# Kernel optimization log

Measured on AMD Instinct MI355X. Metric: run time of the kernel, lower is better.

The kernel has to match this reference:

```python
import jax, jax.numpy as jnp
import numpy as np

DIM = 1024
NUM_HEADS = 16
HEAD_DIM = DIM // NUM_HEADS  # 64
T = 4096
ATTN_SCALE = 0.12


def _rope_tables(t, head_dim):
    # angular_freq: (1/1024)**linspace(0,1,head_dim//4), then zeros for head_dim//4 -> head_dim//2
    af = (1.0 / 1024.0) ** jnp.linspace(0.0, 1.0, head_dim // 4, dtype=jnp.float32)
    af = jnp.concatenate([af, jnp.zeros(head_dim // 4, dtype=jnp.float32)])
    theta = jnp.arange(t, dtype=jnp.float32)[:, None] * af[None, :]  # [T, head_dim//2]
    return jnp.cos(theta), jnp.sin(theta)


def _rms_norm(x):
    eps = jnp.finfo(jnp.float32).eps
    ms = jnp.mean(jnp.square(x.astype(jnp.float32)), axis=-1, keepdims=True)
    return (x * jax.lax.rsqrt(ms + eps)).astype(x.dtype)


def _rotary(x, cos, sin):
    # x: [B, T, H, D]; cos/sin: [T, D//2]
    xf = x.astype(jnp.float32)
    x1, x2 = jnp.split(xf, 2, axis=-1)
    c = cos[None, :, None, :]
    s = sin[None, :, None, :]
    y1 = x1 * c + x2 * s
    y2 = -x1 * s + x2 * c
    return jnp.concatenate([y1, y2], axis=-1).astype(x.dtype)


def setup_inputs() -> dict:
    key = jax.random.key(0)
    k1, k2, k3, k4 = jax.random.split(key, 4)
    std = 0.5 * DIM ** (-0.5)
    bound = (3.0 ** 0.5) * std
    x = jax.random.normal(k1, (1, T, DIM), dtype=jnp.float32)
    ve = jax.random.normal(k2, (1, T, DIM), dtype=jnp.float32)
    qkv_w = jax.random.uniform(k3, (3, DIM, DIM), dtype=jnp.float32, minval=-bound, maxval=bound)
    lambdas = jnp.array([0.5, 0.5], dtype=jnp.float32)
    # source zero-inits c_proj; use random weights for a non-degenerate baseline
    c_proj_w = jax.random.uniform(k4, (DIM, DIM), dtype=jnp.float32, minval=-bound, maxval=bound)
    return {"x": x, "ve": ve, "qkv_w": qkv_w, "lambdas": lambdas, "c_proj_w": c_proj_w}


def reference(x, ve, qkv_w, lambdas, c_proj_w):
    B, t, _ = x.shape
    # fused QKV: F.linear(x, qkv_w.flatten(end_dim=1)) -> [B, T, 3*dim]
    qkv = jnp.einsum('btd,ed->bte', x, qkv_w.reshape(3 * DIM, DIM))
    qkv = qkv.reshape(B, t, 3 * NUM_HEADS, HEAD_DIM)
    q, k, v = jnp.split(qkv, 3, axis=-2)  # each [B, T, H, Dh]
    # lambda-weighted value-embedding mix
    v = lambdas[0] * v + lambdas[1] * ve.reshape(B, t, NUM_HEADS, HEAD_DIM)
    # RMSNorm per head, then RoPE
    q, k = _rms_norm(q), _rms_norm(k)
    cos, sin = _rope_tables(t, HEAD_DIM)
    q, k = _rotary(q, cos, sin), _rotary(k, cos, sin)
    # causal attention with fixed scale (flex_attention w/ causal block mask)
    scores = jnp.einsum('bqhd,bkhd->bhqk', q, k) * ATTN_SCALE
    causal = jnp.tril(jnp.ones((t, t), dtype=bool))
    scores = jnp.where(causal[None, None], scores, jnp.finfo(scores.dtype).min)
    probs = jax.nn.softmax(scores, axis=-1)
    y = jnp.einsum('bhqk,bkhd->bqhd', probs, v).reshape(B, t, DIM)
    return jnp.einsum('btd,ed->bte', y, c_proj_w)
```

## Files before the change

### kernel.cpp

```cpp
#include <hip/hip_runtime.h>
#include <stdint.h>


typedef __attribute__((ext_vector_type(8))) __bf16 bf16x8;
typedef __attribute__((ext_vector_type(8))) unsigned short u16x8;
typedef __attribute__((ext_vector_type(4))) float f32x4;
typedef __attribute__((ext_vector_type(16))) float f32x16;

union U8 { u16x8 s; bf16x8 b; };
union PF { unsigned int u[4]; u16x8 s; bf16x8 b; };

__device__ __forceinline__ float bf2f(unsigned short u) {
  union { unsigned int i; float f; } c; c.i = ((unsigned int)u) << 16; return c.f;
}
__device__ __forceinline__ unsigned short f2bf(float f) {
  union { __bf16 h; unsigned short u; } c; c.h = (__bf16)f; return c.u;
}
__device__ __forceinline__ unsigned int pk2(float lo, float hi) {
  return (unsigned int)f2bf(lo) | ((unsigned int)f2bf(hi) << 16);
}

#define GLOAD16(gp, lp)                                                         \
  __builtin_amdgcn_global_load_lds(                                             \
      (const __attribute__((address_space(1))) void*)(gp),                      \
      (__attribute__((address_space(3))) void*)(lp), 16, 0, 0)

#define MFMA16(a, b, c) __builtin_amdgcn_mfma_f32_16x16x32_bf16((a), (b), (c), 0, 0, 0)
#define MFMA32(a, b, c) __builtin_amdgcn_mfma_f32_32x32x16_bf16((a), (b), (c), 0, 0, 0)

constexpr float ATTN_SCALE = 0.12f;
constexpr float LOG2E = 1.44269504088896340736f;
constexpr float QSCALE = ATTN_SCALE * LOG2E;
constexpr float MFIX = 12.0f;

__global__ void rope_tab(float* __restrict__ ct, float* __restrict__ st) {
  const int i = blockIdx.x * 256 + threadIdx.x;
  if (i >= 4096 * 32) return;
  const int tt = i >> 5, k = i & 31;
  float cv = 1.0f, sv = 0.0f;
  if (k < 16) {
    const float af = powf(1.0f / 1024.0f, (float)k * (1.0f / 15.0f));
    const float th = (float)tt * af;
    cv = cosf(th);
    sv = sinf(th);
  }
  ct[i] = cv; st[i] = sv;
}

__global__ void cast_f2b8(const float* __restrict__ in, unsigned short* __restrict__ out, int n8) {
  const int i = blockIdx.x * 256 + threadIdx.x;
  if (i >= n8) return;
  const float4 a = ((const float4*)in)[2 * i];
  const float4 b = ((const float4*)in)[2 * i + 1];
  u16x8 o;
  o[0] = f2bf(a.x); o[1] = f2bf(a.y); o[2] = f2bf(a.z); o[3] = f2bf(a.w);
  o[4] = f2bf(b.x); o[5] = f2bf(b.y); o[6] = f2bf(b.z); o[7] = f2bf(b.w);
  ((u16x8*)out)[i] = o;
}

template <int OUT_BF16>
__global__ __launch_bounds__(256) void gemm_bt(
    const unsigned short* __restrict__ A, const unsigned short* __restrict__ B,
    void* __restrict__ Cout, int M, int N, int K) {
  __shared__ unsigned short lA[128 * 32];
  __shared__ unsigned short lB[128 * 32];
  const int nbn = N >> 7;
  const int bm = blockIdx.x / nbn, bn = blockIdx.x % nbn;
  const int t = threadIdx.x;
  const int w = t >> 6, l = t & 63;
  const int g = l >> 4, c = l & 15;
  const int wr = (w >> 1) * 64, wc = (w & 1) * 64;

  const int srow = t >> 2;
  const int scol = ((t & 3) << 4) ^ ((srow & 3) << 4);
  const char* ga = (const char*)(A + (size_t)(bm * 128 + srow) * K) + scol;
  const char* gb = (const char*)(B + (size_t)(bn * 128 + srow) * K) + scol;
  const size_t rowK2 = (size_t)64 * K * 2;
  char* la_dst = (char*)lA + t * 16;
  char* lb_dst = (char*)lB + t * 16;

  f32x4 acc[4][4] = {};

  for (int kt = 0; kt < K; kt += 32) {
    const char* gak = ga + (size_t)kt * 2;
    const char* gbk = gb + (size_t)kt * 2;
    GLOAD16(gak, la_dst);
    GLOAD16(gak + rowK2, la_dst + 4096);
    GLOAD16(gbk, lb_dst);
    GLOAD16(gbk + rowK2, lb_dst + 4096);
    __syncthreads();
    U8 af[4], bfr[4];
#pragma unroll
    for (int mi = 0; mi < 4; ++mi) {
      const int row = wr + 16 * mi + c;
      af[mi].s = *(const u16x8*)((const char*)lA + row * 64 + ((16 * g) ^ ((row & 3) << 4)));
    }
#pragma unroll
    for (int ni = 0; ni < 4; ++ni) {
      const int row = wc + 16 * ni + c;
      bfr[ni].s = *(const u16x8*)((const char*)lB + row * 64 + ((16 * g) ^ ((row & 3) << 4)));
    }
#pragma unroll
    for (int mi = 0; mi < 4; ++mi)
#pragma unroll
      for (int ni = 0; ni < 4; ++ni)
        acc[mi][ni] = MFMA16(af[mi].b, bfr[ni].b, acc[mi][ni]);
    __syncthreads();
  }
#pragma unroll
  for (int mi = 0; mi < 4; ++mi) {
#pragma unroll
    for (int ni = 0; ni < 4; ++ni) {
#pragma unroll
      for (int r = 0; r < 4; ++r) {
        const int row = bm * 128 + wr + 16 * mi + 4 * g + r;
        const int col = bn * 128 + wc + 16 * ni + c;
        const float v = acc[mi][ni][r];
        if (OUT_BF16)
          ((unsigned short*)Cout)[(size_t)row * N + col] = f2bf(v);
        else
          ((float*)Cout)[(size_t)row * N + col] = v;
      }
    }
  }
}

__device__ __forceinline__ void load64f(const unsigned short* p, float* x) {
#pragma unroll
  for (int j = 0; j < 8; ++j) {
    const u16x8 v = *(const u16x8*)(p + 8 * j);
#pragma unroll
    for (int e = 0; e < 8; ++e) x[8 * j + e] = bf2f(v[e]);
  }
}

__device__ __forceinline__ void rmsrope_store_blk(const float* x, const float* ct,
                                                  const float* st, unsigned short* outp,
                                                  float pscale) {
  float ms = 0.f;
#pragma unroll
  for (int j = 0; j < 64; ++j) ms += x[j] * x[j];
  const float sc = rsqrtf(ms * (1.0f / 64.0f) + 1.1920928955078125e-7f) * pscale;
  float y[64];
#pragma unroll
  for (int j = 0; j < 32; ++j) {
    const float cc = ct[j], ss = st[j];
    const float a = x[j] * sc, b = x[j + 32] * sc;
    y[j] = a * cc + b * ss;
    y[j + 32] = b * cc - a * ss;
  }
#pragma unroll
  for (int j = 0; j < 8; ++j) {
    u16x8 o;
#pragma unroll
    for (int e = 0; e < 8; ++e) o[e] = f2bf(y[8 * j + e]);
    *(u16x8*)(outp + 256 * j) = o;
  }
}

__global__ __launch_bounds__(256) void fuse_qkv(
    const unsigned short* __restrict__ qkv,
    const float* __restrict__ ve,
    const float* __restrict__ lam,
    const float* __restrict__ ct, const float* __restrict__ st,
    unsigned short* __restrict__ Qb,
    unsigned short* __restrict__ Kb,
    unsigned short* __restrict__ Vb)
{
  __shared__ unsigned short vtile[8][32][65];
  const int b = (int)blockIdx.x;
  const int h = b & 15, tg = b >> 4;
  const int t = threadIdx.x;
  const int g = t >> 5, lq = t & 31;
  const int ti = tg * 8 + g;
  const int tt = ti * 32 + lq;

  const unsigned short* base = qkv + (size_t)tt * 3072 + h * 64;
  const float* ctp = ct + tt * 32;
  const float* stp = st + tt * 32;
  const size_t blk = (size_t)h * 262144 + (size_t)ti * 2048 + lq * 8;

  float x[64];
  load64f(base, x);
  rmsrope_store_blk(x, ctp, stp, Qb + blk, QSCALE);
  load64f(base + 1024, x);
  rmsrope_store_blk(x, ctp, stp, Kb + blk, 1.0f);

  const float l0 = lam[0], l1 = lam[1];
  const float* vp = ve + (size_t)tt * 1024 + h * 64;
  load64f(base + 2048, x);
#pragma unroll
  for (int j = 0; j < 64; ++j) vtile[g][lq][j] = f2bf(l0 * x[j] + l1 * vp[j]);
  __syncthreads();

  unsigned short* vo = Vb + (size_t)h * 262144 + (size_t)ti * 2048 + lq * 8;
#pragma unroll
  for (int r = 0; r < 4; ++r) {
    const int d = lq + 32 * (r & 1);
#pragma unroll
    for (int hi = 0; hi < 2; ++hi) {
      u16x8 o;
#pragma unroll
      for (int j = 0; j < 8; ++j) o[j] = vtile[g][16 * (r >> 1) + 8 * hi + j][d];
      *(u16x8*)(vo + r * 512 + hi * 256) = o;
    }
  }
}

__global__ __launch_bounds__(256, 4) void attn_fa(
    const unsigned short* __restrict__ Qb,
    const unsigned short* __restrict__ Kb,
    const unsigned short* __restrict__ Vb,
    unsigned short* __restrict__ Y)
{
  __shared__ unsigned short oLb[4][64][32];
  __shared__ float sumL[4][32];

  const int b = (int)blockIdx.x;
  const int h = 2 * (b & 7) + ((b >> 3) & 1);
  const int qb = 127 - (b >> 4);
  const int q0 = qb * 32;
  const int t = threadIdx.x;
  const int w = t >> 6, l = t & 63;
  const int lq = l & 31;
  const int hi = l >> 5;

  const unsigned short* kh = Kb + (size_t)h * 262144 + l * 8;
  const unsigned short* vh = Vb + (size_t)h * 262144 + l * 8;

  U8 qf[4];
  {
    const unsigned short* qp = Qb + (size_t)h * 262144 + qb * 2048 + l * 8;
#pragma unroll
    for (int dd = 0; dd < 4; ++dd) qf[dd].s = *(const u16x8*)(qp + dd * 512);
  }

  U8 onesf;
#pragma unroll
  for (int e = 0; e < 8; ++e) onesf.s[e] = 0x3F80;

  f32x16 o0 = {}, o1 = {};
  f32x16 osum = {};

  for (int ti = w; ti <= qb; ti += 4) {
    const unsigned short* kp = kh + ti * 2048;
    const unsigned short* vp = vh + ti * 2048;
    U8 kf[4], vf[4];
#pragma unroll
    for (int dd = 0; dd < 4; ++dd) kf[dd].s = *(const u16x8*)(kp + dd * 512);
#pragma unroll
    for (int r = 0; r < 4; ++r) vf[r].s = *(const u16x8*)(vp + r * 512);

    __builtin_amdgcn_s_setprio(1);
    f32x16 s0 = {};
#pragma unroll
    for (int dd = 0; dd < 4; ++dd) s0 = MFMA32(kf[dd].b, qf[dd].b, s0);
    __builtin_amdgcn_s_setprio(0);

    if (ti == qb) {
      const int thr0 = lq - 4 * hi;
#pragma unroll
      for (int e = 0; e < 16; ++e) {
        const int kvr = (e & 3) + 8 * (e >> 2);
        if (kvr > thr0) s0[e] = -3e38f;
      }
    }

#pragma unroll
    for (int e = 0; e < 16; ++e) s0[e] = exp2f(s0[e] - MFIX);

#define DO_SLAB(KS)                                                              \
  do {                                                                           \
    const unsigned int ua = pk2(s0[8 * (KS) + 0], s0[8 * (KS) + 1]);             \
    const unsigned int ub = pk2(s0[8 * (KS) + 2], s0[8 * (KS) + 3]);             \
    const unsigned int uc = pk2(s0[8 * (KS) + 4], s0[8 * (KS) + 5]);             \
    const unsigned int ud = pk2(s0[8 * (KS) + 6], s0[8 * (KS) + 7]);             \
    const unsigned int sa = (unsigned int)__shfl_xor((int)ua, 32);               \
    const unsigned int sb = (unsigned int)__shfl_xor((int)ub, 32);               \
    const unsigned int sc = (unsigned int)__shfl_xor((int)uc, 32);               \
    const unsigned int sd = (unsigned int)__shfl_xor((int)ud, 32);               \
    PF pf;                                                                       \
    pf.u[0] = hi ? sc : ua;                                                      \
    pf.u[1] = hi ? sd : ub;                                                      \
    pf.u[2] = hi ? uc : sa;                                                      \
    pf.u[3] = hi ? ud : sb;                                                      \
    __builtin_amdgcn_s_setprio(1);                                               \
    o0 = MFMA32(vf[2 * (KS)].b, pf.b, o0);                                       \
    o1 = MFMA32(vf[2 * (KS) + 1].b, pf.b, o1);                                   \
    osum = MFMA32(onesf.b, pf.b, osum);                                          \
    __builtin_amdgcn_s_setprio(0);                                               \
  } while (0)

    DO_SLAB(0);
    DO_SLAB(1);
#undef DO_SLAB
  }

#pragma unroll
  for (int e = 0; e < 16; ++e) {
    const int d = (e & 3) + 8 * (e >> 2) + 4 * hi;
    oLb[w][d][lq] = f2bf(o0[e]);
    oLb[w][d + 32][lq] = f2bf(o1[e]);
  }
  if (hi == 0) sumL[w][lq] = osum[0];
  __syncthreads();

  const int q = t >> 3, dblk = t & 7;
  const float den = sumL[0][q] + sumL[1][q] + sumL[2][q] + sumL[3][q];
  const float invd = 1.0f / den;
  u16x8 yv;
#pragma unroll
  for (int i = 0; i < 8; ++i) {
    const int d = dblk * 8 + i;
    const float a = bf2f(oLb[0][d][q]) + bf2f(oLb[1][d][q]) +
                    bf2f(oLb[2][d][q]) + bf2f(oLb[3][d][q]);
    yv[i] = f2bf(a * invd);
  }
  *(u16x8*)(Y + (size_t)(q0 + q) * 1024 + h * 64 + dblk * 8) = yv;
}

extern "C" void kernel_launch(void* const* d_in, const int* in_sizes, int n_in,
                              void* d_out, int out_size, void* d_ws, size_t ws_size,
                              hipStream_t stream) {
  const float* x   = (const float*)d_in[0];
  const float* ve  = (const float*)d_in[1];
  const float* qw  = (const float*)d_in[2];
  const float* lam = (const float*)d_in[3];
  const float* pw  = (const float*)d_in[4];
  float* out = (float*)d_out;

  unsigned short* ws = (unsigned short*)d_ws;
  unsigned short* x_bf  = ws;
  unsigned short* wqkv  = x_bf + (size_t)4096 * 1024;
  unsigned short* wproj = wqkv + (size_t)3072 * 1024;
  unsigned short* qkv   = wproj + (size_t)1024 * 1024;
  unsigned short* Qb    = qkv + (size_t)4096 * 3072;
  unsigned short* Kb    = Qb + (size_t)4096 * 1024;
  unsigned short* Vb    = Kb + (size_t)4096 * 1024;
  unsigned short* Yb    = Vb + (size_t)4096 * 1024;
  float* ct = (float*)(Yb + (size_t)4096 * 1024);
  float* st = ct + 4096 * 32;

  rope_tab<<<512, 256, 0, stream>>>(ct, st);
  cast_f2b8<<<2048, 256, 0, stream>>>(x, x_bf, 524288);
  cast_f2b8<<<1536, 256, 0, stream>>>(qw, wqkv, 393216);
  cast_f2b8<<<512, 256, 0, stream>>>(pw, wproj, 131072);
  gemm_bt<1><<<768, 256, 0, stream>>>(x_bf, wqkv, (void*)qkv, 4096, 3072, 1024);
  fuse_qkv<<<256, 256, 0, stream>>>(qkv, ve, lam, ct, st, Qb, Kb, Vb);
  attn_fa<<<2048, 256, 0, stream>>>(Qb, Kb, Vb, Yb);
  gemm_bt<0><<<256, 256, 0, stream>>>(Yb, wproj, (void*)out, 4096, 1024, 1024);
}
```

Measured before the change: 165.2 us.

## Fuse prep kernels, remap GEMM blocks across XCDs, drop softmax offset

Merges the rope-table kernel and the three fp32-to-bf16 cast kernels into one launch, which removes three kernel launches and their gaps. Remaps GEMM block IDs so that blocks dispatched round-robin across the 8 XCDs land on contiguous output tiles, which should improve L2 locality. Also removes the constant MFIX subtraction before exp2 in attention. Without that offset the bf16 probabilities and accumulated sums can grow larger, which is a numerical risk.

```diff
diff --git a/kernel.cpp b/kernel.cpp
--- a/kernel.cpp
+++ b/kernel.cpp
@@ -31,31 +31,36 @@
 constexpr float ATTN_SCALE = 0.12f;
 constexpr float LOG2E = 1.44269504088896340736f;
 constexpr float QSCALE = ATTN_SCALE * LOG2E;
-constexpr float MFIX = 12.0f;
-
-__global__ void rope_tab(float* __restrict__ ct, float* __restrict__ st) {
-  const int i = blockIdx.x * 256 + threadIdx.x;
-  if (i >= 4096 * 32) return;
-  const int tt = i >> 5, k = i & 31;
-  float cv = 1.0f, sv = 0.0f;
-  if (k < 16) {
-    const float af = powf(1.0f / 1024.0f, (float)k * (1.0f / 15.0f));
-    const float th = (float)tt * af;
-    cv = cosf(th);
-    sv = sinf(th);
-  }
-  ct[i] = cv; st[i] = sv;
-}
-
-__global__ void cast_f2b8(const float* __restrict__ in, unsigned short* __restrict__ out, int n8) {
-  const int i = blockIdx.x * 256 + threadIdx.x;
-  if (i >= n8) return;
-  const float4 a = ((const float4*)in)[2 * i];
-  const float4 b = ((const float4*)in)[2 * i + 1];
+
+__global__ __launch_bounds__(256) void prep(
+    const float* __restrict__ x, const float* __restrict__ qw,
+    const float* __restrict__ pw, float* __restrict__ ct, float* __restrict__ st,
+    unsigned short* __restrict__ wsbf) {
+  const int b = (int)blockIdx.x;
+  if (b < 512) {
+    const int i = b * 256 + threadIdx.x;
+    const int tt = i >> 5, k = i & 31;
+    float cv = 1.0f, sv = 0.0f;
+    if (k < 16) {
+      const float af = powf(1.0f / 1024.0f, (float)k * (1.0f / 15.0f));
+      const float th = (float)tt * af;
+      cv = cosf(th);
+      sv = sinf(th);
+    }
+    ct[i] = cv; st[i] = sv;
+    return;
+  }
+  const int i8 = (b - 512) * 256 + threadIdx.x;
+  const float* src;
+  if (i8 < 524288) src = x + (size_t)i8 * 8;
+  else if (i8 < 917504) src = qw + (size_t)(i8 - 524288) * 8;
+  else src = pw + (size_t)(i8 - 917504) * 8;
+  const float4 a = ((const float4*)src)[0];
+  const float4 c = ((const float4*)src)[1];
   u16x8 o;
   o[0] = f2bf(a.x); o[1] = f2bf(a.y); o[2] = f2bf(a.z); o[3] = f2bf(a.w);
-  o[4] = f2bf(b.x); o[5] = f2bf(b.y); o[6] = f2bf(b.z); o[7] = f2bf(b.w);
-  ((u16x8*)out)[i] = o;
+  o[4] = f2bf(c.x); o[5] = f2bf(c.y); o[6] = f2bf(c.z); o[7] = f2bf(c.w);
+  ((u16x8*)wsbf)[i8] = o;
 }
 
 template <int OUT_BF16>
@@ -65,7 +70,10 @@
   __shared__ unsigned short lA[128 * 32];
   __shared__ unsigned short lB[128 * 32];
   const int nbn = N >> 7;
-  const int bm = blockIdx.x / nbn, bn = blockIdx.x % nbn;
+  const int cpx = (int)gridDim.x >> 3;
+  const int bid = (int)blockIdx.x;
+  const int sb = (bid & 7) * cpx + (bid >> 3);
+  const int bm = sb / nbn, bn = sb % nbn;
   const int t = threadIdx.x;
   const int w = t >> 6, l = t & 63;
   const int g = l >> 4, c = l & 15;
@@ -267,7 +275,7 @@
     }
 
 #pragma unroll
-    for (int e = 0; e < 16; ++e) s0[e] = exp2f(s0[e] - MFIX);
+    for (int e = 0; e < 16; ++e) s0[e] = exp2f(s0[e]);
 
 #define DO_SLAB(KS)                                                              \
   do {                                                                           \
@@ -341,10 +349,7 @@
   float* ct = (float*)(Yb + (size_t)4096 * 1024);
   float* st = ct + 4096 * 32;
 
-  rope_tab<<<512, 256, 0, stream>>>(ct, st);
-  cast_f2b8<<<2048, 256, 0, stream>>>(x, x_bf, 524288);
-  cast_f2b8<<<1536, 256, 0, stream>>>(qw, wqkv, 393216);
-  cast_f2b8<<<512, 256, 0, stream>>>(pw, wproj, 131072);
+  prep<<<4608, 256, 0, stream>>>(x, qw, pw, ct, st, ws);
   gemm_bt<1><<<768, 256, 0, stream>>>(x_bf, wqkv, (void*)qkv, 4096, 3072, 1024);
   fuse_qkv<<<256, 256, 0, stream>>>(qkv, ve, lam, ct, st, Qb, Kb, Vb);
   attn_fa<<<2048, 256, 0, stream>>>(Qb, Kb, Vb, Yb);
```

Measured after the change: 154.8 us. 6.3% less time.
